# Performance work log

Hardware: AMD Instinct MI355X
Metric: run time of the kernel (lower is better)

## Reference

```python
import math
import jax, jax.numpy as jnp
import numpy as np

LAMBDA_INIT = 0.8
GN_EPS = 1e-5

B, H, S, D = 2, 16, 2048, 128  # batch, heads, seq, head_dim


def setup_inputs() -> dict:
    key = jax.random.key(0)
    ks = jax.random.split(key, 8)
    return {
        "q": jax.random.normal(ks[0], (B, H, S, 2 * D), dtype=jnp.float32),
        "k": jax.random.normal(ks[1], (B, H, S, 2 * D), dtype=jnp.float32),
        "v": jax.random.normal(ks[2], (B, H, S, D), dtype=jnp.float32),
        "lam_q1": jax.random.normal(ks[3], (D,), dtype=jnp.float32),
        "lam_q2": jax.random.normal(ks[4], (D,), dtype=jnp.float32),
        "lam_k1": jax.random.normal(ks[5], (D,), dtype=jnp.float32),
        "lam_k2": jax.random.normal(ks[6], (D,), dtype=jnp.float32),
        "gn_weight": jnp.ones((H * D,), dtype=jnp.float32),
        "gn_bias": jnp.zeros((H * D,), dtype=jnp.float32),
    }


def reference(q, k, v, lam_q1, lam_q2, lam_k1, lam_k2, gn_weight, gn_bias):
    d = q.shape[-1] // 2
    scale = 1.0 / math.sqrt(d)
    Q1, Q2 = q[..., :d], q[..., d:]
    K1, K2 = k[..., :d], k[..., d:]
    # dual score matrices [B,H,S,S]
    w1 = jax.nn.softmax(jnp.einsum('bhsd,bhtd->bhst', Q1, K1) * scale, axis=-1)
    w2 = jax.nn.softmax(jnp.einsum('bhsd,bhtd->bhst', Q2, K2) * scale, axis=-1)
    lam = jnp.exp(jnp.dot(lam_q1, lam_k1)) - jnp.exp(jnp.dot(lam_q2, lam_k2)) + LAMBDA_INIT
    weights = w1 - lam * w2
    out = jnp.einsum('bhst,bhtd->bhsd', weights, v)  # [B,H,S,D]
    # GroupNorm(num_groups=H, num_channels=H*D) applied on [B, H*D, S]:
    # channel c = h*D + dd, normalization per (batch, head) over (D, S).
    mean = out.mean(axis=(2, 3), keepdims=True)
    var = out.var(axis=(2, 3), keepdims=True)
    normed = (out - mean) * jax.lax.rsqrt(var + GN_EPS)
    gamma = gn_weight.reshape(1, out.shape[1], 1, d)
    beta = gn_bias.reshape(1, out.shape[1], 1, d)
    return (normed * gamma + beta) * (1.0 - LAMBDA_INIT)
```

## Files before the change

### kernel.cpp

```cpp
#include <hip/hip_runtime.h>
#include <cstddef>

constexpr int B = 2, H = 16, S = 2048, D = 128;
constexpr int BH = B * H;
constexpr int TWOD = 2 * D;
constexpr int QTILE = 128;
constexpr int BC = 32;
constexpr int NKT = S / BC;
constexpr float SC2 = 0.08838834764831845f * 1.4426950408889634f;
constexpr float LAM_INIT = 0.8f;
constexpr float GN_EPS = 1e-5f;

typedef __attribute__((ext_vector_type(8))) short short8;
typedef __attribute__((ext_vector_type(4))) float f32x4;

__device__ __forceinline__ unsigned short f2b(float f) {
  unsigned int u = __float_as_uint(f);
  u += 0x7fffu + ((u >> 16) & 1u);
  return (unsigned short)(u >> 16);
}

__device__ __forceinline__ void async_copy16(const void* g, void* l) {
  typedef __attribute__((address_space(1))) const void gvoid;
  typedef __attribute__((address_space(3))) void lvoid;
  __builtin_amdgcn_global_load_lds((gvoid*)g, (lvoid*)l, 16, 0, 0);
}

__global__ void prep_kernel(const float* __restrict__ k, const float* __restrict__ v,
                            const float* __restrict__ lq1, const float* __restrict__ lq2,
                            const float* __restrict__ lk1, const float* __restrict__ lk2,
                            unsigned short* __restrict__ kbf, unsigned short* __restrict__ vtg,
                            float* __restrict__ wsf) {
  __shared__ float tile[64][129];
  const int bh = blockIdx.y, s0 = blockIdx.x * 64, t = threadIdx.x;

  if (blockIdx.x == 0 && blockIdx.y == 0) {
    if (t < 128) {
      tile[0][t] = lq1[t] * lk1[t];
      tile[1][t] = lq2[t] * lk2[t];
    }
    __syncthreads();
    if (t == 0) {
      float s1 = 0.f, s2 = 0.f;
      for (int i = 0; i < 128; ++i) { s1 += tile[0][i]; s2 += tile[1][i]; }
      wsf[0] = expf(s1) - expf(s2) + LAM_INIT;
    }
    __syncthreads();
  }

  {
    const float* ks = k + ((size_t)bh * S + s0) * TWOD;
    unsigned short* kd = kbf + ((size_t)bh * S + s0) * TWOD;
#pragma unroll
    for (int i = 0; i < 8; ++i) {
      size_t off = (size_t)(i * 256 + t) * 8;
      float4 a = *(const float4*)(ks + off);
      float4 b2 = *(const float4*)(ks + off + 4);
      unsigned short u[8];
      u[0] = f2b(a.x); u[1] = f2b(a.y); u[2] = f2b(a.z); u[3] = f2b(a.w);
      u[4] = f2b(b2.x); u[5] = f2b(b2.y); u[6] = f2b(b2.z); u[7] = f2b(b2.w);
      *(uint4*)(kd + off) = *(uint4*)u;
    }
  }

#pragma unroll
  for (int i = 0; i < 8; ++i) {
    int idx = t + i * 256;
    int row = idx >> 5, c4 = idx & 31;
    float4 f = *(const float4*)(v + ((size_t)bh * S + s0 + row) * D + c4 * 4);
    tile[row][c4 * 4 + 0] = f.x; tile[row][c4 * 4 + 1] = f.y;
    tile[row][c4 * 4 + 2] = f.z; tile[row][c4 * 4 + 3] = f.w;
  }
  __syncthreads();
#pragma unroll
  for (int i = 0; i < 4; ++i) {
    int c = t + i * 256;
    int d = c >> 3, k8 = c & 7;
    unsigned short u[8];
#pragma unroll
    for (int j = 0; j < 8; ++j) u[j] = f2b(tile[k8 * 8 + j][d]);
    *(uint4*)(vtg + ((size_t)bh * D + d) * S + s0 + k8 * 8) = *(uint4*)u;
  }
}

__global__ __launch_bounds__(256, 2)
void attn_kernel(const float* __restrict__ q, const unsigned short* __restrict__ kbf,
                 const unsigned short* __restrict__ vtg,
                 float* __restrict__ wsf, float* __restrict__ out) {
  __shared__ __attribute__((aligned(16))) unsigned short Ks[2][8192];
  __shared__ __attribute__((aligned(16))) unsigned short Vt3[3][4096];
  __shared__ __attribute__((aligned(16))) unsigned short Pa[4][2][32][40];
  __shared__ float sred[4][2];

  const int bh = blockIdx.x, qb = blockIdx.y;
  const int q0 = qb * QTILE;
  const int tid = threadIdx.x;
  const int wave = tid >> 6, lane = tid & 63;
  const int quad = lane >> 4, l16 = lane & 15;
  const float lam = wsf[0];

  short8 qf[2][2][4];
#pragma unroll
  for (int mt = 0; mt < 2; ++mt) {
    int qrow = q0 + wave * 32 + mt * 16 + l16;
    const float* qr = q + ((size_t)bh * S + qrow) * TWOD;
#pragma unroll
    for (int st = 0; st < 2; ++st)
#pragma unroll
      for (int ks = 0; ks < 4; ++ks) {
        const float* p = qr + st * D + ks * 32 + quad * 8;
        float4 f0 = *(const float4*)p;
        float4 f1 = *(const float4*)(p + 4);
        short8 v8;
        v8[0] = (short)f2b(f0.x); v8[1] = (short)f2b(f0.y);
        v8[2] = (short)f2b(f0.z); v8[3] = (short)f2b(f0.w);
        v8[4] = (short)f2b(f1.x); v8[5] = (short)f2b(f1.y);
        v8[6] = (short)f2b(f1.z); v8[7] = (short)f2b(f1.w);
        qf[mt][st][ks] = v8;
      }
  }

  int koff[4];
#pragma unroll
  for (int j = 0; j < 4; ++j) {
    int L = j * 64 + lane;
    int row = L >> 5, cs = L & 31;
    koff[j] = row * 256 + (cs ^ (row & 7)) * 8;
  }
  int voff;
  {
    int d = lane >> 2, cs = lane & 3;
    voff = d * S + (cs ^ (d & 3)) * 8;
  }
  const unsigned short* kbase = kbf + (size_t)bh * S * (size_t)TWOD;
  const unsigned short* vbase = vtg + (size_t)bh * D * (size_t)S;

  f32x4 acc[2][2][8];
#pragma unroll
  for (int mt = 0; mt < 2; ++mt)
#pragma unroll
    for (int st = 0; st < 2; ++st)
#pragma unroll
      for (int n = 0; n < 8; ++n) acc[mt][st][n] = (f32x4){0.f, 0.f, 0.f, 0.f};
  float lacc[2][2][4];
#pragma unroll
  for (int mt = 0; mt < 2; ++mt)
#pragma unroll
    for (int st = 0; st < 2; ++st)
#pragma unroll
      for (int r = 0; r < 4; ++r) lacc[mt][st][r] = 0.f;

  const int pa_rd_off = (quad ^ ((l16 >> 2) & 3)) * 8;
  const int vro = l16 * 32 + ((quad ^ (l16 & 3)) * 8);

  auto qk = [&](int st, int kb, f32x4 (&sa)[2][2]) {
#pragma unroll
    for (int nt = 0; nt < 2; ++nt) {
      const int row = nt * 16 + l16;
      const int rx = row & 7;
#pragma unroll
      for (int ks = 0; ks < 4; ++ks) {
        const int pos = (st * 16 + ks * 4 + quad) ^ rx;
        const short8 kf = *(const short8*)&Ks[kb][row * 256 + pos * 8];
        sa[0][nt] = __builtin_amdgcn_mfma_f32_16x16x32_bf16(qf[0][st][ks], kf, sa[0][nt], 0, 0, 0);
        sa[1][nt] = __builtin_amdgcn_mfma_f32_16x16x32_bf16(qf[1][st][ks], kf, sa[1][nt], 0, 0, 0);
      }
    }
  };
  auto pexp = [&](int st, f32x4 (&sa)[2][2]) {
#pragma unroll
    for (int mt = 0; mt < 2; ++mt)
#pragma unroll
      for (int nt = 0; nt < 2; ++nt)
#pragma unroll
        for (int r = 0; r < 4; ++r) {
          float p = __builtin_amdgcn_exp2f(sa[mt][nt][r] * SC2);
          lacc[mt][st][r] += p;
          int colp = (((nt * 2) + (l16 >> 3)) ^ quad) * 8 + (l16 & 7);
          Pa[wave][st][mt * 16 + quad * 4 + r][colp] = f2b(p);
        }
  };
  auto pv = [&](int st, const short8 (&paf)[2], const short8 (&vf)[8]) {
#pragma unroll
    for (int nt8 = 0; nt8 < 8; ++nt8)
#pragma unroll
      for (int mt = 0; mt < 2; ++mt)
        acc[mt][st][nt8] = __builtin_amdgcn_mfma_f32_16x16x32_bf16(paf[mt], vf[nt8], acc[mt][st][nt8], 0, 0, 0);
  };
  auto dma_tile = [&](int t, unsigned short* kd, unsigned short* vd) {
    const unsigned short* kp = kbase + (size_t)t * BC * TWOD;
#pragma unroll
    for (int j = 0; j < 16; ++j)
      async_copy16(kp + koff[j & 3] + (j >> 2) * 2048, kd + j * 512);
    const unsigned short* vp = vbase + t * BC;
#pragma unroll
    for (int j = 0; j < 8; ++j)
      async_copy16(vp + voff + j * 16 * S, vd + j * 512);
  };

  {
    const uint4 z = {0u, 0u, 0u, 0u};
    unsigned short* pz = &Pa[0][0][0][0];
    for (int i = tid; i < 1280; i += 256) *(uint4*)(pz + i * 8) = z;
    unsigned short* vz = &Vt3[2][0];
    for (int i = tid; i < 512; i += 256) *(uint4*)(vz + i * 8) = z;
    dma_tile(0, &Ks[0][0], &Vt3[0][0]);
  }
  __syncthreads();

  int vw = 1, vr = 2;
  for (int t = 0; t < NKT; ++t) {
    asm volatile("s_waitcnt lgkmcnt(0)" ::: "memory");
    __builtin_amdgcn_s_barrier();

    const int kb = t & 1;
    if (t + 1 < NKT) {
      dma_tile(t + 1, &Ks[kb ^ 1][0], &Vt3[vw][0]);
      asm volatile("s_waitcnt vmcnt(24)" ::: "memory");
    } else {
      asm volatile("s_waitcnt vmcnt(0)" ::: "memory");
    }

    short8 vf[8], paf[2][2];
    const unsigned short* vc = &Vt3[vr][0];
#pragma unroll
    for (int nt8 = 0; nt8 < 8; ++nt8)
      vf[nt8] = *(const short8*)&vc[nt8 * 512 + vro];
#pragma unroll
    for (int st = 0; st < 2; ++st)
#pragma unroll
      for (int mt = 0; mt < 2; ++mt)
        paf[st][mt] = *(const short8*)&Pa[wave][st][mt * 16 + l16][pa_rd_off];

    f32x4 sa0[2][2], sa1[2][2];
#pragma unroll
    for (int mt = 0; mt < 2; ++mt)
#pragma unroll
      for (int nt = 0; nt < 2; ++nt) {
        sa0[mt][nt] = (f32x4){0.f, 0.f, 0.f, 0.f};
        sa1[mt][nt] = (f32x4){0.f, 0.f, 0.f, 0.f};
      }
    qk(0, kb, sa0);
    pv(0, paf[0], vf);
    pexp(0, sa0);
    qk(1, kb, sa1);
    pv(1, paf[1], vf);
    pexp(1, sa1);

    vw = (vw == 2) ? 0 : vw + 1;
    vr = (vr == 2) ? 0 : vr + 1;
  }

  {
    short8 paf[2][2], vf[8];
    const unsigned short* vc = &Vt3[vr][0];
#pragma unroll
    for (int nt8 = 0; nt8 < 8; ++nt8)
      vf[nt8] = *(const short8*)&vc[nt8 * 512 + vro];
#pragma unroll
    for (int st = 0; st < 2; ++st)
#pragma unroll
      for (int mt = 0; mt < 2; ++mt)
        paf[st][mt] = *(const short8*)&Pa[wave][st][mt * 16 + l16][pa_rd_off];
    pv(0, paf[0], vf);
    pv(1, paf[1], vf);
  }

#pragma unroll
  for (int mt = 0; mt < 2; ++mt)
#pragma unroll
    for (int st = 0; st < 2; ++st)
#pragma unroll
      for (int r = 0; r < 4; ++r) {
        float v = lacc[mt][st][r];
        v += __shfl_xor(v, 1, 16);
        v += __shfl_xor(v, 2, 16);
        v += __shfl_xor(v, 4, 16);
        v += __shfl_xor(v, 8, 16);
        lacc[mt][st][r] = v;
      }

  float sum = 0.f, ssq = 0.f;
#pragma unroll
  for (int mt = 0; mt < 2; ++mt) {
    float i1[4], i2[4];
#pragma unroll
    for (int r = 0; r < 4; ++r) {
      i1[r] = 1.f / lacc[mt][0][r];
      i2[r] = lam / lacc[mt][1][r];
    }
#pragma unroll
    for (int nt8 = 0; nt8 < 8; ++nt8)
#pragma unroll
      for (int r = 0; r < 4; ++r) {
        float o = acc[mt][0][nt8][r] * i1[r] - acc[mt][1][nt8][r] * i2[r];
        int row = q0 + wave * 32 + mt * 16 + quad * 4 + r;
        out[((size_t)bh * S + row) * D + nt8 * 16 + l16] = o;
        sum += o; ssq += o * o;
      }
  }
#pragma unroll
  for (int off = 32; off >= 1; off >>= 1) {
    sum += __shfl_xor(sum, off, 64);
    ssq += __shfl_xor(ssq, off, 64);
  }
  if (lane == 0) { sred[wave][0] = sum; sred[wave][1] = ssq; }
  __syncthreads();
  if (tid == 0) {
    float s0 = sred[0][0] + sred[1][0] + sred[2][0] + sred[3][0];
    float s1 = sred[0][1] + sred[1][1] + sred[2][1] + sred[3][1];
    int idx = bh * 16 + qb;
    wsf[64 + idx * 2] = s0;
    wsf[64 + idx * 2 + 1] = s1;
  }
}

__global__ void gn_kernel(float* __restrict__ out, const float* __restrict__ gw,
                          const float* __restrict__ gb, const float* __restrict__ wsf) {
  const int bh = blockIdx.x, part = blockIdx.y;
  const int h = bh & (H - 1);
  float sum = 0.f, ssq = 0.f;
  for (int j = 0; j < 16; ++j) {
    sum += wsf[64 + (bh * 16 + j) * 2];
    ssq += wsf[64 + (bh * 16 + j) * 2 + 1];
  }
  const float invn = 1.f / (float)(S * D);
  const float mean = sum * invn;
  const float var = ssq * invn - mean * mean;
  const float rstd = rsqrtf(var + GN_EPS);
  const float outscale = 1.f - LAM_INIT;
  const float4* g4 = (const float4*)(gw + h * D);
  const float4* b4 = (const float4*)(gb + h * D);
  float4* o4 = (float4*)(out + (size_t)bh * S * D);
  const int chunks_per = (S * D / 4) / 32;
  const int c0 = part * chunks_per;
  for (int c = c0 + threadIdx.x; c < c0 + chunks_per; c += 256) {
    float4 vv = o4[c];
    int d4 = c & 31;
    float4 g = g4[d4], bb = b4[d4];
    vv.x = ((vv.x - mean) * rstd * g.x + bb.x) * outscale;
    vv.y = ((vv.y - mean) * rstd * g.y + bb.y) * outscale;
    vv.z = ((vv.z - mean) * rstd * g.z + bb.z) * outscale;
    vv.w = ((vv.w - mean) * rstd * g.w + bb.w) * outscale;
    o4[c] = vv;
  }
}

extern "C" void kernel_launch(void* const* d_in, const int* in_sizes, int n_in,
                              void* d_out, int out_size, void* d_ws, size_t ws_size,
                              hipStream_t stream) {
  (void)in_sizes; (void)n_in; (void)out_size; (void)ws_size;
  const float* q   = (const float*)d_in[0];
  const float* k   = (const float*)d_in[1];
  const float* v   = (const float*)d_in[2];
  const float* lq1 = (const float*)d_in[3];
  const float* lq2 = (const float*)d_in[4];
  const float* lk1 = (const float*)d_in[5];
  const float* lk2 = (const float*)d_in[6];
  const float* gw  = (const float*)d_in[7];
  const float* gb  = (const float*)d_in[8];
  float* out = (float*)d_out;
  float* wsf = (float*)d_ws;
  unsigned short* vtg = (unsigned short*)((char*)d_ws + 8192);
  unsigned short* kbf = (unsigned short*)((char*)d_ws + 8192 + (size_t)BH * D * S * 2);

  prep_kernel<<<dim3(S / 64, BH), dim3(256), 0, stream>>>(k, v, lq1, lq2, lk1, lk2, kbf, vtg, wsf);
  attn_kernel<<<dim3(BH, S / QTILE), dim3(256), 0, stream>>>(q, kbf, vtg, wsf, out);
  gn_kernel<<<dim3(BH, 32), dim3(256), 0, stream>>>(out, gw, gb, wsf);
}
```

Baseline: 455.5 us.

## Split K/V tile async copies across waves and enlarge prep tiles

```diff
diff --git a/kernel.cpp b/kernel.cpp
--- a/kernel.cpp
+++ b/kernel.cpp
@@ -31,8 +31,8 @@
                             const float* __restrict__ lk1, const float* __restrict__ lk2,
                             unsigned short* __restrict__ kbf, unsigned short* __restrict__ vtg,
                             float* __restrict__ wsf) {
-  __shared__ float tile[64][129];
-  const int bh = blockIdx.y, s0 = blockIdx.x * 64, t = threadIdx.x;
+  __shared__ float tile[128][129];
+  const int bh = blockIdx.y, s0 = blockIdx.x * 128, t = threadIdx.x;
 
   if (blockIdx.x == 0 && blockIdx.y == 0) {
     if (t < 128) {
@@ -52,7 +52,7 @@
     const float* ks = k + ((size_t)bh * S + s0) * TWOD;
     unsigned short* kd = kbf + ((size_t)bh * S + s0) * TWOD;
 #pragma unroll
-    for (int i = 0; i < 8; ++i) {
+    for (int i = 0; i < 16; ++i) {
       size_t off = (size_t)(i * 256 + t) * 8;
       float4 a = *(const float4*)(ks + off);
       float4 b2 = *(const float4*)(ks + off + 4);
@@ -64,7 +64,7 @@
   }
 
 #pragma unroll
-  for (int i = 0; i < 8; ++i) {
+  for (int i = 0; i < 16; ++i) {
     int idx = t + i * 256;
     int row = idx >> 5, c4 = idx & 31;
     float4 f = *(const float4*)(v + ((size_t)bh * S + s0 + row) * D + c4 * 4);
@@ -73,9 +73,9 @@
   }
   __syncthreads();
 #pragma unroll
-  for (int i = 0; i < 4; ++i) {
+  for (int i = 0; i < 8; ++i) {
     int c = t + i * 256;
-    int d = c >> 3, k8 = c & 7;
+    int d = c >> 4, k8 = c & 15;
     unsigned short u[8];
 #pragma unroll
     for (int j = 0; j < 8; ++j) u[j] = f2b(tile[k8 * 8 + j][d]);
@@ -97,7 +97,9 @@
   const int tid = threadIdx.x;
   const int wave = tid >> 6, lane = tid & 63;
   const int quad = lane >> 4, l16 = lane & 15;
+
   const float lam = wsf[0];
+  asm volatile("" :: "v"(lam));
 
   short8 qf[2][2][4];
 #pragma unroll
@@ -120,17 +122,21 @@
       }
   }
 
-  int koff[4];
-#pragma unroll
-  for (int j = 0; j < 4; ++j) {
-    int L = j * 64 + lane;
-    int row = L >> 5, cs = L & 31;
-    koff[j] = row * 256 + (cs ^ (row & 7)) * 8;
-  }
-  int voff;
-  {
-    int d = lane >> 2, cs = lane & 3;
-    voff = d * S + (cs ^ (d & 3)) * 8;
+  int ksrc[4], kdst[4];
+#pragma unroll
+  for (int i = 0; i < 4; ++i) {
+    int chunk = wave * 256 + i * 64 + lane;
+    int row = chunk >> 5, cs = lane & 31;
+    ksrc[i] = row * 256 + (cs ^ (row & 7)) * 8;
+    kdst[i] = chunk * 8;
+  }
+  int vsrc[2], vdst[2];
+#pragma unroll
+  for (int i = 0; i < 2; ++i) {
+    int chunk = wave * 128 + i * 64 + lane;
+    int d = chunk >> 2, cs = lane & 3;
+    vsrc[i] = d * S + (cs ^ (d & 3)) * 8;
+    vdst[i] = chunk * 8;
   }
   const unsigned short* kbase = kbf + (size_t)bh * S * (size_t)TWOD;
   const unsigned short* vbase = vtg + (size_t)bh * D * (size_t)S;
@@ -190,12 +196,12 @@
   auto dma_tile = [&](int t, unsigned short* kd, unsigned short* vd) {
     const unsigned short* kp = kbase + (size_t)t * BC * TWOD;
 #pragma unroll
-    for (int j = 0; j < 16; ++j)
-      async_copy16(kp + koff[j & 3] + (j >> 2) * 2048, kd + j * 512);
+    for (int i = 0; i < 4; ++i)
+      async_copy16(kp + ksrc[i], kd + kdst[i]);
     const unsigned short* vp = vbase + t * BC;
 #pragma unroll
-    for (int j = 0; j < 8; ++j)
-      async_copy16(vp + voff + j * 16 * S, vd + j * 512);
+    for (int i = 0; i < 2; ++i)
+      async_copy16(vp + vsrc[i], vd + vdst[i]);
   };
 
   {
@@ -206,23 +212,21 @@
     for (int i = tid; i < 512; i += 256) *(uint4*)(vz + i * 8) = z;
     dma_tile(0, &Ks[0][0], &Vt3[0][0]);
   }
-  __syncthreads();
-
-  int vw = 1, vr = 2;
+
   for (int t = 0; t < NKT; ++t) {
     asm volatile("s_waitcnt lgkmcnt(0)" ::: "memory");
     __builtin_amdgcn_s_barrier();
 
-    const int kb = t & 1;
     if (t + 1 < NKT) {
-      dma_tile(t + 1, &Ks[kb ^ 1][0], &Vt3[vw][0]);
-      asm volatile("s_waitcnt vmcnt(24)" ::: "memory");
+      dma_tile(t + 1, &Ks[(t + 1) & 1][0], &Vt3[(t + 1) % 3][0]);
+      asm volatile("s_waitcnt vmcnt(6)" ::: "memory");
     } else {
       asm volatile("s_waitcnt vmcnt(0)" ::: "memory");
     }
+    __builtin_amdgcn_s_barrier();
 
     short8 vf[8], paf[2][2];
-    const unsigned short* vc = &Vt3[vr][0];
+    const unsigned short* vc = &Vt3[(t + 2) % 3][0];
 #pragma unroll
     for (int nt8 = 0; nt8 < 8; ++nt8)
       vf[nt8] = *(const short8*)&vc[nt8 * 512 + vro];
@@ -240,20 +244,18 @@
         sa0[mt][nt] = (f32x4){0.f, 0.f, 0.f, 0.f};
         sa1[mt][nt] = (f32x4){0.f, 0.f, 0.f, 0.f};
       }
+    const int kb = t & 1;
     qk(0, kb, sa0);
     pv(0, paf[0], vf);
     pexp(0, sa0);
     qk(1, kb, sa1);
     pv(1, paf[1], vf);
     pexp(1, sa1);
-
-    vw = (vw == 2) ? 0 : vw + 1;
-    vr = (vr == 2) ? 0 : vr + 1;
   }
 
   {
     short8 paf[2][2], vf[8];
-    const unsigned short* vc = &Vt3[vr][0];
+    const unsigned short* vc = &Vt3[(NKT - 1) % 3][0];
 #pragma unroll
     for (int nt8 = 0; nt8 < 8; ++nt8)
       vf[nt8] = *(const short8*)&vc[nt8 * 512 + vro];
@@ -364,7 +366,7 @@
   unsigned short* vtg = (unsigned short*)((char*)d_ws + 8192);
   unsigned short* kbf = (unsigned short*)((char*)d_ws + 8192 + (size_t)BH * D * S * 2);
 
-  prep_kernel<<<dim3(S / 64, BH), dim3(256), 0, stream>>>(k, v, lq1, lq2, lk1, lk2, kbf, vtg, wsf);
+  prep_kernel<<<dim3(S / 128, BH), dim3(256), 0, stream>>>(k, v, lq1, lq2, lk1, lk2, kbf, vtg, wsf);
   attn_kernel<<<dim3(BH, S / QTILE), dim3(256), 0, stream>>>(q, kbf, vtg, wsf, out);
   gn_kernel<<<dim3(BH, 32), dim3(256), 0, stream>>>(out, gw, gb, wsf);
 }
```

New measurement: 433.7 us. 4.8% less time.
